# Performance work log

Hardware: AMD Instinct MI355X
Metric: run time of the kernel (lower is better)

## Reference

```python
import jax, jax.numpy as jnp
import numpy as np
from functools import partial

OBS_DIM = 128
HID = 256
DENSE = [512, 512]
ACT_DIM = 32
B, S = 256, 512


def _lin(key, fan_in, fan_out, scale=0.02):
    kw, kb = jax.random.split(key)
    W = jax.random.normal(kw, (fan_in, fan_out), jnp.float32) * scale
    b = jnp.zeros((fan_out,), jnp.float32)
    return W, b


def setup_inputs() -> dict:
    key = jax.random.key(0)
    ks = jax.random.split(key, 16)
    obs = jax.random.normal(ks[0], (B, S, OBS_DIM), jnp.float32)
    action = jax.random.randint(ks[1], (B,), 0, ACT_DIM)
    comb = OBS_DIM + HID
    Wf, bf = _lin(ks[2], comb, HID)
    Wi, bi = _lin(ks[3], comb, HID)
    Wc, bc = _lin(ks[4], comb, HID)
    Wo, bo = _lin(ks[5], comb, HID)
    W1, b1 = _lin(ks[6], HID, DENSE[0])
    W2, b2 = _lin(ks[7], DENSE[0], DENSE[1])
    A1, a1 = _lin(ks[8], DENSE[1], 64)
    A2, a2 = _lin(ks[9], 64, 64)
    A3, a3 = _lin(ks[10], 64, ACT_DIM, scale=0.01)
    C1, c1 = _lin(ks[11], DENSE[1], 64)
    C2, c2 = _lin(ks[12], 64, 64)
    C3, c3 = _lin(ks[13], 64, 1)
    return dict(obs=obs, action=action, Wf=Wf, bf=bf, Wi=Wi, bi=bi, Wc=Wc, bc=bc,
                Wo=Wo, bo=bo, W1=W1, b1=b1, W2=W2, b2=b2,
                A1=A1, a1=a1, A2=A2, a2=a2, A3=A3, a3=a3,
                C1=C1, c1=c1, C2=C2, c2=c2, C3=C3, c3=c3)


def _forward(obs, action, Wf, bf, Wi, bi, Wc, bc, Wo, bo,
             W1, b1, W2, b2, A1, a1, A2, a2, A3, a3, C1, c1, C2, c2, C3, c3):
    Bn, Sn, _ = obs.shape
    h0 = jnp.zeros((Bn, HID), obs.dtype)
    c0 = jnp.zeros((Bn, HID), obs.dtype)

    def step(carry, x_t):  # x_t: [B, obs_dim]
        h, c = carry
        comb = jnp.concatenate([x_t, h], axis=1)  # [B, obs+hid]
        f_g = jax.nn.sigmoid(comb @ Wf + bf)
        i_g = jax.nn.sigmoid(comb @ Wi + bi)
        c_g = jnp.tanh(comb @ Wc + bc)
        o_g = jax.nn.sigmoid(comb @ Wo + bo)
        c_new = f_g * c + i_g * c_g
        h_new = o_g * jnp.tanh(c_new)
        return (h_new, c_new), h_new

    xs = jnp.swapaxes(obs, 0, 1)  # [S, B, obs_dim]
    (_, _), hs = jax.lax.scan(step, (h0, c0), xs)
    emb = jnp.swapaxes(hs, 0, 1)  # [B, S, HID]

    z = jax.nn.relu(emb @ W1 + b1)
    z = jax.nn.relu(z @ W2 + b2)  # [B, S, DENSE[-1]]
    e = z[:, -1, :]  # last timestep embedding [B, DENSE[-1]]

    a = jnp.tanh(e @ A1 + a1)
    a = jnp.tanh(a @ A2 + a2)
    logits = a @ A3 + a3  # [B, ACT_DIM]

    v = jnp.tanh(e @ C1 + c1)
    v = jnp.tanh(v @ C2 + c2)
    values = (v @ C3 + c3).squeeze(-1)  # [B]

    logp_all = jax.nn.log_softmax(logits, axis=-1)
    logp = jnp.take_along_axis(logp_all, action[:, None], axis=1).squeeze(-1)
    entropy = -jnp.sum(jnp.exp(logp_all) * logp_all, axis=-1)
    return jnp.stack([logp, entropy, values], axis=0)  # [3, B]


def reference(obs, action, Wf, bf, Wi, bi, Wc, bc, Wo, bo,
              W1, b1, W2, b2, A1, a1, A2, a2, A3, a3, C1, c1, C2, c2, C3, c3):
    return _forward(obs, action, Wf, bf, Wi, bi, Wc, bc, Wo, bo,
                    W1, b1, W2, b2, A1, a1, A2, a2, A3, a3,
                    C1, c1, C2, c2, C3, c3)
```

## Files before the change

kernel.cpp:

```cpp
#include <hip/hip_runtime.h>
#include <cstddef>


#define S_LEN 512
#define OBS_D 128
#define HIDN  256
#define BATCH 256
#define ROWS  8
#define NWG   32
#define ACT_DIM 32
#define CSTRIDE 400
#define GSTRIDE 1028

typedef float f32x4 __attribute__((ext_vector_type(4)));

#define L2E 1.4426950408889634f

__device__ __forceinline__ float sigexp2(float y) {
    return __builtin_amdgcn_rcpf(1.0f + __builtin_amdgcn_exp2f(-y));
}

__global__ void __launch_bounds__(512, 2)
lstm_fused(const float* __restrict__ obs,
           const float* __restrict__ Wfp, const float* __restrict__ bfp,
           const float* __restrict__ Wip, const float* __restrict__ bip,
           const float* __restrict__ Wcp, const float* __restrict__ bcp,
           const float* __restrict__ Wop, const float* __restrict__ bop,
           float* __restrict__ hfinal)
{
    __shared__ __align__(16) unsigned char comb[16][CSTRIDE];
    __shared__ __align__(16) float gates[ROWS][GSTRIDE];
    __shared__ float biasL[1024];

    const int tid  = threadIdx.x;
    const int wv   = tid >> 6;
    const int lane = tid & 63;
    const int l15  = lane & 15, lg = lane >> 4;
    const int b0   = blockIdx.x * ROWS;

    {
        const float* Bg[4] = { bfp, bip, bcp, bop };
        for (int c = tid; c < 1024; c += 512) {
            const int g = c >> 8;
            biasL[c] = Bg[g][c & 255] * ((g == 2) ? 2.0f * L2E : L2E);
        }
    }
    for (int i = tid; i < 16 * CSTRIDE / 4; i += 512)
        ((int*)comb)[i] = 0;

    long long wfrag[8][12];
    {
        const float* Wg[4] = { Wfp, Wip, Wcp, Wop };
#pragma unroll
        for (int tile = 0; tile < 8; ++tile) {
            const int col = wv * 128 + tile * 16 + l15;
            const float* src = Wg[col >> 8] + (col & 255);
#pragma unroll
            for (int kk = 0; kk < 12; ++kk) {
                const int k0 = kk * 32 + lg * 8;
                int lo = 0, hi = 0;
                lo = __builtin_amdgcn_cvt_pk_fp8_f32(
                        src[(size_t)(k0 + 0) * HIDN] * 16.f,
                        src[(size_t)(k0 + 1) * HIDN] * 16.f, lo, false);
                lo = __builtin_amdgcn_cvt_pk_fp8_f32(
                        src[(size_t)(k0 + 2) * HIDN] * 16.f,
                        src[(size_t)(k0 + 3) * HIDN] * 16.f, lo, true);
                hi = __builtin_amdgcn_cvt_pk_fp8_f32(
                        src[(size_t)(k0 + 4) * HIDN] * 16.f,
                        src[(size_t)(k0 + 5) * HIDN] * 16.f, hi, false);
                hi = __builtin_amdgcn_cvt_pk_fp8_f32(
                        src[(size_t)(k0 + 6) * HIDN] * 16.f,
                        src[(size_t)(k0 + 7) * HIDN] * 16.f, hi, true);
                wfrag[tile][kk] = (long long)(unsigned)lo | ((long long)hi << 32);
            }
        }
    }

    f32x4 creg = { 0.f, 0.f, 0.f, 0.f };

    const float* xbase = obs + (size_t)(b0 + wv) * S_LEN * OBS_D + 2 * lane;
    float2 xv = *(const float2*)(xbase);

    __syncthreads();

#pragma unroll 1
    for (int t = 0; t < S_LEN; ++t) {
        {
            const int p = __builtin_amdgcn_cvt_pk_fp8_f32(xv.x, xv.y, 0, false);
            *(short*)(&comb[wv][2 * lane]) = (short)p;
        }
        const int tn = (t + 1 < S_LEN) ? t + 1 : t;
        xv = *(const float2*)(xbase + (size_t)tn * OBS_D);
        __syncthreads();

        f32x4 acc[8];
#pragma unroll
        for (int i = 0; i < 8; ++i) acc[i] = (f32x4){ 0.f, 0.f, 0.f, 0.f };
#pragma unroll
        for (int kk = 0; kk < 12; ++kk) {
            const long long a = *(const long long*)(&comb[l15][kk * 32 + lg * 8]);
#pragma unroll
            for (int tile = 0; tile < 8; ++tile)
                acc[tile] = __builtin_amdgcn_mfma_f32_16x16x32_fp8_fp8(
                                a, wfrag[tile][kk], acc[tile], 0, 0, 0);
        }

        if (lg < 2) {
#pragma unroll
            for (int tile = 0; tile < 8; ++tile) {
                const int col = wv * 128 + tile * 16 + l15;
                const float sg = ((col >> 8) == 2 ? 2.0f * L2E : L2E) * 0.0625f;
                const float bs = biasL[col];
#pragma unroll
                for (int q = 0; q < 4; ++q)
                    gates[lg * 4 + q][col] = fmaf(acc[tile][q], sg, bs);
            }
        }
        __syncthreads();

        {
            const f32x4 yf = *(const f32x4*)(&gates[wv][      4 * lane]);
            const f32x4 yi = *(const f32x4*)(&gates[wv][256 + 4 * lane]);
            const f32x4 yc = *(const f32x4*)(&gates[wv][512 + 4 * lane]);
            const f32x4 yo = *(const f32x4*)(&gates[wv][768 + 4 * lane]);
            f32x4 hv;
#pragma unroll
            for (int u = 0; u < 4; ++u) {
                const float f  = sigexp2(yf[u]);
                const float i  = sigexp2(yi[u]);
                const float cg = 2.0f * sigexp2(yc[u]) - 1.0f;
                const float o  = sigexp2(yo[u]);
                creg[u] = f * creg[u] + i * cg;
                const float th = 2.0f * sigexp2(2.0f * L2E * creg[u]) - 1.0f;
                hv[u] = o * th;
            }
            int p = __builtin_amdgcn_cvt_pk_fp8_f32(hv[0], hv[1], 0, false);
            p     = __builtin_amdgcn_cvt_pk_fp8_f32(hv[2], hv[3], p, true);
            *(int*)(&comb[wv][OBS_D + 4 * lane]) = p;
            if (t == S_LEN - 1)
                *(f32x4*)(&hfinal[(size_t)(b0 + wv) * HIDN + 4 * lane]) = hv;
        }
    }
}

__device__ __forceinline__ float tanh_f(float x) {
    return 2.0f / (1.0f + __expf(-2.0f * x)) - 1.0f;
}

__global__ void __launch_bounds__(256)
head_kernel(const float* __restrict__ hfin,
            const float* __restrict__ W1, const float* __restrict__ b1v,
            const float* __restrict__ W2, const float* __restrict__ b2v,
            const float* __restrict__ A1, const float* __restrict__ a1v,
            const float* __restrict__ A2, const float* __restrict__ a2v,
            const float* __restrict__ A3, const float* __restrict__ a3v,
            const float* __restrict__ C1, const float* __restrict__ c1v,
            const float* __restrict__ C2, const float* __restrict__ c2v,
            const float* __restrict__ C3, const float* __restrict__ c3v,
            const int* __restrict__ action,
            float* __restrict__ out)
{
    __shared__ float e0[4][HIDN];
    __shared__ float z1s[4][512];
    __shared__ float z2s[4][512];
    __shared__ float aL[4][64], vL[4][64], a2L[4][64], v2L[4][64];
    __shared__ float lgL[4][ACT_DIM];
    __shared__ float valL[4];

    const int tid = threadIdx.x;
    const int b0 = blockIdx.x * 4;

    for (int idx = tid; idx < 4 * HIDN; idx += 256) {
        const int r = idx >> 8, k = idx & 255;
        e0[r][k] = hfin[(size_t)(b0 + r) * HIDN + k];
    }
    __syncthreads();

    for (int i = 0; i < 8; ++i) {
        const int idx = i * 256 + tid;
        const int r = idx >> 9, cc = idx & 511;
        float acc = b1v[cc];
#pragma unroll 8
        for (int k = 0; k < HIDN; ++k) acc = fmaf(e0[r][k], W1[k * 512 + cc], acc);
        z1s[r][cc] = fmaxf(acc, 0.0f);
    }
    __syncthreads();

    for (int i = 0; i < 8; ++i) {
        const int idx = i * 256 + tid;
        const int r = idx >> 9, cc = idx & 511;
        float acc = b2v[cc];
#pragma unroll 8
        for (int k = 0; k < 512; ++k) acc = fmaf(z1s[r][k], W2[k * 512 + cc], acc);
        z2s[r][cc] = fmaxf(acc, 0.0f);
    }
    __syncthreads();

    {
        const int r = tid >> 6, j = tid & 63;
        float acc = a1v[j], accv = c1v[j];
#pragma unroll 8
        for (int k = 0; k < 512; ++k) {
            const float e = z2s[r][k];
            acc  = fmaf(e, A1[k * 64 + j], acc);
            accv = fmaf(e, C1[k * 64 + j], accv);
        }
        aL[r][j] = tanh_f(acc);
        vL[r][j] = tanh_f(accv);
    }
    __syncthreads();
    {
        const int r = tid >> 6, j = tid & 63;
        float acc = a2v[j], accv = c2v[j];
#pragma unroll 8
        for (int k = 0; k < 64; ++k) {
            acc  = fmaf(aL[r][k], A2[k * 64 + j], acc);
            accv = fmaf(vL[r][k], C2[k * 64 + j], accv);
        }
        a2L[r][j] = tanh_f(acc);
        v2L[r][j] = tanh_f(accv);
    }
    __syncthreads();
    if (tid < 128) {
        const int r = tid >> 5, j = tid & 31;
        float acc = a3v[j];
#pragma unroll 8
        for (int k = 0; k < 64; ++k) acc = fmaf(a2L[r][k], A3[k * ACT_DIM + j], acc);
        lgL[r][j] = acc;
    }
    if (tid >= 128 && tid < 132) {
        const int r = tid - 128;
        float acc = c3v[0];
#pragma unroll 8
        for (int k = 0; k < 64; ++k) acc = fmaf(v2L[r][k], C3[k], acc);
        valL[r] = acc;
    }
    __syncthreads();

    {
        const int wv = tid >> 6, lane = tid & 63;
        const float x = (lane < ACT_DIM) ? lgL[wv][lane] : -3.4e38f;
        float m = x;
        for (int off = 32; off; off >>= 1) m = fmaxf(m, __shfl_xor(m, off));
        const float p = (lane < ACT_DIM) ? __expf(x - m) : 0.0f;
        float s = p;
        for (int off = 32; off; off >>= 1) s += __shfl_xor(s, off);
        const float logs = logf(s);
        const float lp = x - m - logs;
        const int act = action[b0 + wv];
        float sel = (lane == act) ? lp : 0.0f;
        for (int off = 32; off; off >>= 1) sel += __shfl_xor(sel, off);
        float et = (lane < ACT_DIM) ? p * lp : 0.0f;
        for (int off = 32; off; off >>= 1) et += __shfl_xor(et, off);
        if (lane == 0) {
            const int b = b0 + wv;
            out[b]             = sel;
            out[BATCH + b]     = -et / s;
            out[2 * BATCH + b] = valL[wv];
        }
    }
}

extern "C" void kernel_launch(void* const* d_in, const int* in_sizes, int n_in,
                              void* d_out, int out_size, void* d_ws, size_t ws_size,
                              hipStream_t stream) {
    const float* obs = (const float*)d_in[0];
    const int*   action = (const int*)d_in[1];
    const float* Wfp = (const float*)d_in[2];  const float* bfp = (const float*)d_in[3];
    const float* Wip = (const float*)d_in[4];  const float* bip = (const float*)d_in[5];
    const float* Wcp = (const float*)d_in[6];  const float* bcp = (const float*)d_in[7];
    const float* Wop = (const float*)d_in[8];  const float* bop = (const float*)d_in[9];
    const float* W1  = (const float*)d_in[10]; const float* b1v = (const float*)d_in[11];
    const float* W2  = (const float*)d_in[12]; const float* b2v = (const float*)d_in[13];
    const float* A1  = (const float*)d_in[14]; const float* a1v = (const float*)d_in[15];
    const float* A2  = (const float*)d_in[16]; const float* a2v = (const float*)d_in[17];
    const float* A3  = (const float*)d_in[18]; const float* a3v = (const float*)d_in[19];
    const float* C1  = (const float*)d_in[20]; const float* c1v = (const float*)d_in[21];
    const float* C2  = (const float*)d_in[22]; const float* c2v = (const float*)d_in[23];
    const float* C3  = (const float*)d_in[24]; const float* c3v = (const float*)d_in[25];

    float* hfinal = (float*)d_ws;

    lstm_fused<<<dim3(NWG), dim3(512), 0, stream>>>(
        obs, Wfp, bfp, Wip, bip, Wcp, bcp, Wop, bop, hfinal);

    head_kernel<<<dim3(64), dim3(256), 0, stream>>>(
        hfinal, W1, b1v, W2, b2v, A1, a1v, A2, a2v, A3, a3v,
        C1, c1v, C2, c2v, C3, c3v, action, (float*)d_out);
}
```

Before: 1.662 ms.

## Switch LSTM recurrence to int8 MFMA with column-split gates and double-buffered LDS

Replaces the fp8 16x16x32 MFMA recurrence with int8 16x16x64 MFMA. Each wave now owns 32 hidden units across all four gates, so the gate nonlinearities run directly from accumulators and the separate gates LDS round trip and one barrier per step are dropped. The output-gate weights are moved to LDS to relieve register pressure. Obs and h are double-buffered in LDS, and the next obs row is staged by idle lanes during the matmul. The cost is lower precision: fixed-scale int8 quantization of weights, h and obs clamps values and may hurt accuracy.

```diff
diff --git a/kernel.cpp b/kernel.cpp
--- a/kernel.cpp
+++ b/kernel.cpp
@@ -9,16 +9,30 @@
 #define ROWS  8
 #define NWG   32
 #define ACT_DIM 32
-#define CSTRIDE 400
-#define GSTRIDE 1028
-
+
+#define XW_OFF   0
+#define XW_BYTES (16 * 16 * 400)
+#define XB_OFF   XW_BYTES
+#define XB_BYTES (2 * 16 * 144)
+#define HB_OFF   (XB_OFF + XB_BYTES)
+#define HB_BYTES (2 * 16 * 272)
+#define LDS_TOTAL (HB_OFF + HB_BYTES)
+
+typedef int   i32x4 __attribute__((ext_vector_type(4)));
 typedef float f32x4 __attribute__((ext_vector_type(4)));
 
 #define L2E 1.4426950408889634f
+#define DQS (L2E / 32768.0f)
 
 __device__ __forceinline__ float sigexp2(float y) {
     return __builtin_amdgcn_rcpf(1.0f + __builtin_amdgcn_exp2f(-y));
 }
+__device__ __forceinline__ int q8(float v) {
+    float c = fmaxf(-127.0f, fminf(127.0f, v));
+    return ((int)__builtin_rintf(c)) & 255;
+}
+
+extern __shared__ char smem[];
 
 __global__ void __launch_bounds__(512, 2)
 lstm_fused(const float* __restrict__ obs,
@@ -28,10 +42,6 @@
            const float* __restrict__ Wop, const float* __restrict__ bop,
            float* __restrict__ hfinal)
 {
-    __shared__ __align__(16) unsigned char comb[16][CSTRIDE];
-    __shared__ __align__(16) float gates[ROWS][GSTRIDE];
-    __shared__ float biasL[1024];
-
     const int tid  = threadIdx.x;
     const int wv   = tid >> 6;
     const int lane = tid & 63;
@@ -39,107 +49,139 @@
     const int b0   = blockIdx.x * ROWS;
 
     {
-        const float* Bg[4] = { bfp, bip, bcp, bop };
-        for (int c = tid; c < 1024; c += 512) {
-            const int g = c >> 8;
-            biasL[c] = Bg[g][c & 255] * ((g == 2) ? 2.0f * L2E : L2E);
-        }
-    }
-    for (int i = tid; i < 16 * CSTRIDE / 4; i += 512)
-        ((int*)comb)[i] = 0;
-
-    long long wfrag[8][12];
-    {
-        const float* Wg[4] = { Wfp, Wip, Wcp, Wop };
-#pragma unroll
-        for (int tile = 0; tile < 8; ++tile) {
-            const int col = wv * 128 + tile * 16 + l15;
-            const float* src = Wg[col >> 8] + (col & 255);
-#pragma unroll
-            for (int kk = 0; kk < 12; ++kk) {
-                const int k0 = kk * 32 + lg * 8;
-                int lo = 0, hi = 0;
-                lo = __builtin_amdgcn_cvt_pk_fp8_f32(
-                        src[(size_t)(k0 + 0) * HIDN] * 16.f,
-                        src[(size_t)(k0 + 1) * HIDN] * 16.f, lo, false);
-                lo = __builtin_amdgcn_cvt_pk_fp8_f32(
-                        src[(size_t)(k0 + 2) * HIDN] * 16.f,
-                        src[(size_t)(k0 + 3) * HIDN] * 16.f, lo, true);
-                hi = __builtin_amdgcn_cvt_pk_fp8_f32(
-                        src[(size_t)(k0 + 4) * HIDN] * 16.f,
-                        src[(size_t)(k0 + 5) * HIDN] * 16.f, hi, false);
-                hi = __builtin_amdgcn_cvt_pk_fp8_f32(
-                        src[(size_t)(k0 + 6) * HIDN] * 16.f,
-                        src[(size_t)(k0 + 7) * HIDN] * 16.f, hi, true);
-                wfrag[tile][kk] = (long long)(unsigned)lo | ((long long)hi << 32);
+        int* zp = (int*)(smem + XB_OFF);
+        for (int i = tid; i < (XB_BYTES + HB_BYTES) / 4; i += 512) zp[i] = 0;
+    }
+    {
+#pragma unroll
+        for (int u = 0; u < 2; ++u) {
+            const int col = wv * 32 + u * 16 + l15;
+            const float* src = Wop + col;
+            char* dst = smem + XW_OFF + (size_t)(wv * 2 + u) * 6400
+                      + l15 * 400 + lg * 96;
+#pragma unroll
+            for (int j = 0; j < 24; ++j) {
+                const int k0 = lg * 96 + j * 4;
+                const int b = q8(src[(size_t)(k0 + 0) * HIDN] * 1024.f)
+                           | (q8(src[(size_t)(k0 + 1) * HIDN] * 1024.f) << 8)
+                           | (q8(src[(size_t)(k0 + 2) * HIDN] * 1024.f) << 16)
+                           | (q8(src[(size_t)(k0 + 3) * HIDN] * 1024.f) << 24);
+                *(int*)(dst + j * 4) = b;
             }
         }
     }
 
-    f32x4 creg = { 0.f, 0.f, 0.f, 0.f };
-
-    const float* xbase = obs + (size_t)(b0 + wv) * S_LEN * OBS_D + 2 * lane;
-    float2 xv = *(const float2*)(xbase);
-
+    i32x4 wfr[6][6];
+#pragma unroll
+    for (int tt = 0; tt < 6; ++tt) {
+        const int g = tt >> 1, jt = tt & 1;
+        const int col = wv * 32 + jt * 16 + l15;
+        const float* src = ((g == 0) ? Wfp : (g == 1) ? Wip : Wcp) + col;
+#pragma unroll
+        for (int kk = 0; kk < 6; ++kk) {
+            i32x4 v;
+#pragma unroll
+            for (int w = 0; w < 4; ++w) {
+                const int k0 = kk * 64 + lg * 16 + w * 4;
+                v[w] = q8(src[(size_t)(k0 + 0) * HIDN] * 1024.f)
+                     | (q8(src[(size_t)(k0 + 1) * HIDN] * 1024.f) << 8)
+                     | (q8(src[(size_t)(k0 + 2) * HIDN] * 1024.f) << 16)
+                     | (q8(src[(size_t)(k0 + 3) * HIDN] * 1024.f) << 24);
+            }
+            wfr[tt][kk] = v;
+        }
+    }
+
+    float bF[2], bI[2], bC[2], bO[2];
+#pragma unroll
+    for (int jt = 0; jt < 2; ++jt) {
+        const int u = wv * 32 + jt * 16 + l15;
+        bF[jt] = bfp[u] * L2E;
+        bI[jt] = bip[u] * L2E;
+        bC[jt] = bcp[u] * (2.0f * L2E);
+        bO[jt] = bop[u] * L2E;
+    }
+
+    f32x4 cr0 = {0.f, 0.f, 0.f, 0.f};
+    f32x4 cr1 = {0.f, 0.f, 0.f, 0.f};
+
+    __syncthreads();
+
+    const int isStager = (lg >= 2);
+    const int sidx = (lg - 2) * 16 + l15;
+    const float* xsrc = obs + (size_t)(b0 + wv) * S_LEN * OBS_D + sidx * 4;
+    float4 xv = {0.f, 0.f, 0.f, 0.f};
+    if (isStager) {
+        const float4 x0 = *(const float4*)(xsrc);
+        const int qp = q8(x0.x * 32.f) | (q8(x0.y * 32.f) << 8)
+                     | (q8(x0.z * 32.f) << 16) | (q8(x0.w * 32.f) << 24);
+        *(int*)(smem + XB_OFF + wv * 144 + sidx * 4) = qp;
+        xv = *(const float4*)(xsrc + OBS_D);
+    }
     __syncthreads();
 
 #pragma unroll 1
     for (int t = 0; t < S_LEN; ++t) {
-        {
-            const int p = __builtin_amdgcn_cvt_pk_fp8_f32(xv.x, xv.y, 0, false);
-            *(short*)(&comb[wv][2 * lane]) = (short)p;
-        }
-        const int tn = (t + 1 < S_LEN) ? t + 1 : t;
-        xv = *(const float2*)(xbase + (size_t)tn * OBS_D);
+        const int p = t & 1;
+        const char* xrow = smem + XB_OFF + p * 2304 + l15 * 144 + lg * 16;
+        const char* hrow = smem + HB_OFF + p * 4352 + l15 * 272 + lg * 16;
+        const char* wl   = smem + XW_OFF + (size_t)wv * 12800 + l15 * 400 + lg * 16;
+
+        i32x4 acc[8];
+#pragma unroll
+        for (int i2 = 0; i2 < 8; ++i2) acc[i2] = (i32x4){0, 0, 0, 0};
+
+#pragma unroll
+        for (int kk = 0; kk < 6; ++kk) {
+            const i32x4 a = (kk < 2) ? *(const i32x4*)(xrow + kk * 64)
+                                     : *(const i32x4*)(hrow + (kk - 2) * 64);
+            const i32x4 b6 = *(const i32x4*)(wl + kk * 64);
+            const i32x4 b7 = *(const i32x4*)(wl + 6400 + kk * 64);
+            acc[0] = __builtin_amdgcn_mfma_i32_16x16x64_i8(a, wfr[0][kk], acc[0], 0, 0, 0);
+            acc[1] = __builtin_amdgcn_mfma_i32_16x16x64_i8(a, wfr[1][kk], acc[1], 0, 0, 0);
+            acc[2] = __builtin_amdgcn_mfma_i32_16x16x64_i8(a, wfr[2][kk], acc[2], 0, 0, 0);
+            acc[3] = __builtin_amdgcn_mfma_i32_16x16x64_i8(a, wfr[3][kk], acc[3], 0, 0, 0);
+            acc[4] = __builtin_amdgcn_mfma_i32_16x16x64_i8(a, wfr[4][kk], acc[4], 0, 0, 0);
+            acc[5] = __builtin_amdgcn_mfma_i32_16x16x64_i8(a, wfr[5][kk], acc[5], 0, 0, 0);
+            acc[6] = __builtin_amdgcn_mfma_i32_16x16x64_i8(a, b6, acc[6], 0, 0, 0);
+            acc[7] = __builtin_amdgcn_mfma_i32_16x16x64_i8(a, b7, acc[7], 0, 0, 0);
+        }
+
+        if (isStager) {
+            const int qp = q8(xv.x * 32.f) | (q8(xv.y * 32.f) << 8)
+                         | (q8(xv.z * 32.f) << 16) | (q8(xv.w * 32.f) << 24);
+            *(int*)(smem + XB_OFF + (p ^ 1) * 2304 + wv * 144 + sidx * 4) = qp;
+            if (t + 2 < S_LEN)
+                xv = *(const float4*)(xsrc + (size_t)(t + 2) * OBS_D);
+        } else {
+#pragma unroll
+            for (int jt = 0; jt < 2; ++jt) {
+#pragma unroll
+                for (int q = 0; q < 4; ++q) {
+                    const float yf = fmaf((float)acc[0 + jt][q], DQS, bF[jt]);
+                    const float yi = fmaf((float)acc[2 + jt][q], DQS, bI[jt]);
+                    const float yc = fmaf((float)acc[4 + jt][q], 2.0f * DQS, bC[jt]);
+                    const float yo = fmaf((float)acc[6 + jt][q], DQS, bO[jt]);
+                    const float fv = sigexp2(yf);
+                    const float iv = sigexp2(yi);
+                    const float cv = 2.0f * sigexp2(yc) - 1.0f;
+                    const float ov = sigexp2(yo);
+                    float c = (jt ? cr1[q] : cr0[q]);
+                    c = fv * c + iv * cv;
+                    if (jt) cr1[q] = c; else cr0[q] = c;
+                    const float th = 2.0f * sigexp2(2.0f * L2E * c) - 1.0f;
+                    const float hv = ov * th;
+                    const int row = lg * 4 + q;
+                    const int hq = ((int)__builtin_rintf(hv * 32.0f)) & 255;
+                    *(unsigned char*)(smem + HB_OFF + (p ^ 1) * 4352
+                                      + row * 272 + wv * 32 + jt * 16 + l15)
+                        = (unsigned char)hq;
+                    if (t == S_LEN - 1)
+                        hfinal[(size_t)(b0 + row) * HIDN + wv * 32 + jt * 16 + l15] = hv;
+                }
+            }
+        }
         __syncthreads();
-
-        f32x4 acc[8];
-#pragma unroll
-        for (int i = 0; i < 8; ++i) acc[i] = (f32x4){ 0.f, 0.f, 0.f, 0.f };
-#pragma unroll
-        for (int kk = 0; kk < 12; ++kk) {
-            const long long a = *(const long long*)(&comb[l15][kk * 32 + lg * 8]);
-#pragma unroll
-            for (int tile = 0; tile < 8; ++tile)
-                acc[tile] = __builtin_amdgcn_mfma_f32_16x16x32_fp8_fp8(
-                                a, wfrag[tile][kk], acc[tile], 0, 0, 0);
-        }
-
-        if (lg < 2) {
-#pragma unroll
-            for (int tile = 0; tile < 8; ++tile) {
-                const int col = wv * 128 + tile * 16 + l15;
-                const float sg = ((col >> 8) == 2 ? 2.0f * L2E : L2E) * 0.0625f;
-                const float bs = biasL[col];
-#pragma unroll
-                for (int q = 0; q < 4; ++q)
-                    gates[lg * 4 + q][col] = fmaf(acc[tile][q], sg, bs);
-            }
-        }
-        __syncthreads();
-
-        {
-            const f32x4 yf = *(const f32x4*)(&gates[wv][      4 * lane]);
-            const f32x4 yi = *(const f32x4*)(&gates[wv][256 + 4 * lane]);
-            const f32x4 yc = *(const f32x4*)(&gates[wv][512 + 4 * lane]);
-            const f32x4 yo = *(const f32x4*)(&gates[wv][768 + 4 * lane]);
-            f32x4 hv;
-#pragma unroll
-            for (int u = 0; u < 4; ++u) {
-                const float f  = sigexp2(yf[u]);
-                const float i  = sigexp2(yi[u]);
-                const float cg = 2.0f * sigexp2(yc[u]) - 1.0f;
-                const float o  = sigexp2(yo[u]);
-                creg[u] = f * creg[u] + i * cg;
-                const float th = 2.0f * sigexp2(2.0f * L2E * creg[u]) - 1.0f;
-                hv[u] = o * th;
-            }
-            int p = __builtin_amdgcn_cvt_pk_fp8_f32(hv[0], hv[1], 0, false);
-            p     = __builtin_amdgcn_cvt_pk_fp8_f32(hv[2], hv[3], p, true);
-            *(int*)(&comb[wv][OBS_D + 4 * lane]) = p;
-            if (t == S_LEN - 1)
-                *(f32x4*)(&hfinal[(size_t)(b0 + wv) * HIDN + 4 * lane]) = hv;
-        }
     }
 }
 
@@ -281,7 +323,10 @@
 
     float* hfinal = (float*)d_ws;
 
-    lstm_fused<<<dim3(NWG), dim3(512), 0, stream>>>(
+    hipFuncSetAttribute((const void*)lstm_fused,
+                        hipFuncAttributeMaxDynamicSharedMemorySize, LDS_TOTAL);
+
+    lstm_fused<<<dim3(NWG), dim3(512), LDS_TOTAL, stream>>>(
         obs, Wfp, bfp, Wip, bip, Wcp, bcp, Wop, bop, hfinal);
 
     head_kernel<<<dim3(64), dim3(256), 0, stream>>>(
```

New measurement: 1.663 ms. No clear change (+0.1%).
